# Kernel tuning notes

Measured on AMD Instinct MI355X. Metric: run time of the kernel, lower is better.

## Reference

```python
import jax, jax.numpy as jnp
import numpy as np

# NLMConv1DBlock: NLM LogicMachine(depth=2, breadth=2, input_dims=[0, inp_dim, 3],
# output_dims=[D,D,D], logic_hidden_dim=None -> each logic MLP is Linear+Sigmoid),
# followed by swish -> Conv1d(D, D, k=3, pad=1) over the t axis -> swish.
# Only the unary (arity-1) output of the second NLM layer is consumed, so the
# nullary/binary heads of layer 2 are never computed (their params are unused).


def swish(x):
    return x * jax.nn.sigmoid(x)


def lin_sig(x, W, b):
    # LogicInference with logic_hidden_dim=None: single Linear + Sigmoid
    return jax.nn.sigmoid(x @ W.T + b)


def reduce_unary(f1):
    # Reducer(dim=1): [B, n, C] -> [B, 2C]; exclude_self is a no-op for arity 1.
    # Channels interleaved as (exists_0, forall_0, exists_1, forall_1, ...)
    e = jnp.max(f1, axis=1)
    a = jnp.min(f1, axis=1)
    return jnp.stack([e, a], axis=-1).reshape(f1.shape[0], -1)


def reduce_pair(f2):
    # Reducer(dim=2, exclude_self=True): [B, n, n, C] -> [B, n, 2C].
    # Diagonal (i==j) masked to 0 for exists(max) and 1 for forall(min);
    # reduction over the second object index (axis=2). Interleaved exists/forall.
    n = f2.shape[1]
    eye = jnp.eye(n, dtype=bool)[None, :, :, None]
    e = jnp.max(jnp.where(eye, jnp.zeros((), f2.dtype), f2), axis=2)
    a = jnp.min(jnp.where(eye, jnp.ones((), f2.dtype), f2), axis=2)
    return jnp.stack([e, a], axis=-1).reshape(f2.shape[0], n, -1)


def perm2(f2):
    # Permutation(dim=2): concat identity and object-dim transpose along channels
    return jnp.concatenate([f2, jnp.swapaxes(f2, 1, 2)], axis=-1)


def setup_inputs() -> dict:
    key = jax.random.key(0)
    ks = jax.random.split(key, 12)
    b, t, n, inp_dim, D = 16, 16, 64, 2, 32
    s = 0.1
    x = jax.random.normal(ks[0], (b, t, n, inp_dim), jnp.float32)
    # Layer 1 logic MLPs (forward concat order: [expand, input, reduce])
    W1_0 = jax.random.normal(ks[1], (D, 2 * inp_dim), jnp.float32) * s        # nullary: reduce(unary) -> 2*inp_dim
    b1_0 = jax.random.normal(ks[2], (D,), jnp.float32) * s
    W1_1 = jax.random.normal(ks[3], (D, inp_dim + 6), jnp.float32) * s        # unary: [x, reduce(cmp)] -> inp_dim + 2*3
    b1_1 = jax.random.normal(ks[4], (D,), jnp.float32) * s
    W1_2 = jax.random.normal(ks[5], (D, 2 * (inp_dim + 3)), jnp.float32) * s  # binary: perm2([expand(x), cmp])
    b1_2 = jax.random.normal(ks[6], (D,), jnp.float32) * s
    # Layer 2, only the unary head is used downstream
    W2_1 = jax.random.normal(ks[7], (D, 4 * D), jnp.float32) * s              # [expand(g0), g1, reduce(g2)]
    b2_1 = jax.random.normal(ks[8], (D,), jnp.float32) * s
    # Conv1d(D, D, kernel_size=3, padding=1), OIH layout
    Wc = jax.random.normal(ks[9], (D, D, 3), jnp.float32) * s
    bc = jax.random.normal(ks[10], (D,), jnp.float32) * s
    return {"x": x, "W1_0": W1_0, "b1_0": b1_0, "W1_1": W1_1, "b1_1": b1_1,
            "W1_2": W1_2, "b1_2": b1_2, "W2_1": W2_1, "b2_1": b2_1,
            "Wc": Wc, "bc": bc}


def reference(x, W1_0, b1_0, W1_1, b1_1, W1_2, b1_2, W2_1, b2_1, Wc, bc):
    b, t, n, c = x.shape
    B = b * t
    xf = x.reshape(B, n, c)

    # pairwise relational inputs: [B, n, n, 3]
    ar = jnp.arange(n)
    base = jnp.stack([ar[:, None] < ar[None, :], ar[:, None] == ar[None, :]],
                     axis=-1).astype(x.dtype)                       # [n, n, 2], batch-invariant
    numbers = xf[:, :, 1]
    cmp3 = (numbers[:, :, None] < numbers[:, None, :]).astype(x.dtype)
    cmp = jnp.concatenate([jnp.broadcast_to(base[None], (B, n, n, 2)),
                           cmp3[..., None]], axis=-1)

    # --- NLM layer 1 (input dims [0, c, 3]) ---
    g0 = lin_sig(reduce_unary(xf), W1_0, b1_0)                                # [B, D]
    g1 = lin_sig(jnp.concatenate([xf, reduce_pair(cmp)], axis=-1), W1_1, b1_1)  # [B, n, D]
    f2 = jnp.concatenate([jnp.broadcast_to(xf[:, :, None, :], (B, n, n, c)), cmp], axis=-1)
    g2 = lin_sig(perm2(f2), W1_2, b1_2)                                       # [B, n, n, D]

    # --- NLM layer 2, unary head only (block takes nlm(...)[1]) ---
    D = g1.shape[-1]
    h1_in = jnp.concatenate([jnp.broadcast_to(g0[:, None, :], (B, n, D)),
                             g1, reduce_pair(g2)], axis=-1)                   # [B, n, 4D]
    h1 = swish(lin_sig(h1_in, W2_1, b2_1))                                    # [B, n, D]

    # (b t) n c -> (b n) c t, conv1d over t, -> b t n c, swish
    y = h1.reshape(b, t, n, D).transpose(0, 2, 3, 1).reshape(b * n, D, t)
    y = jax.lax.conv_general_dilated(y, Wc, (1,), [(1, 1)],
                                     dimension_numbers=('NCH', 'OIH', 'NCH'))
    y = y + bc[None, :, None]
    y = y.reshape(b, n, D, t).transpose(0, 3, 1, 2)
    return swish(y)
```

## Files before the change

kernel.cpp:

```cpp
#include <hip/hip_runtime.h>

#define NN 64
#define DD 32

__device__ __forceinline__ float sigmoidf_(float x) {
    return 1.0f / (1.0f + __expf(-x));
}

__global__ __launch_bounds__(1024) void stage1_kernel(
    const float* __restrict__ x,
    const float* __restrict__ W1_0, const float* __restrict__ b1_0,
    const float* __restrict__ W1_1, const float* __restrict__ b1_1,
    const float* __restrict__ W1_2, const float* __restrict__ b1_2,
    const float* __restrict__ W2_1, const float* __restrict__ b2_1,
    float* __restrict__ h1ws)
{
    __shared__ __align__(16) float sx0[NN];
    __shared__ __align__(16) float sx1[NN];
    __shared__ __align__(16) float sBvT[DD][68];
    __shared__ __align__(16) float sFeat[NN][100];
    __shared__ __align__(16) float sW2p[DD][100];
    __shared__ float sW12[DD*10];
    __shared__ float sB12[DD];
    __shared__ float sW11t[8*DD];
    __shared__ float sB11[DD];
    __shared__ float sG0[DD];
    __shared__ float sZ0[DD];
    __shared__ float sEC2[NN];
    __shared__ float sAC2[NN];

    const int tid = threadIdx.x;
    const int bb  = blockIdx.x;
    const int d   = tid & 31;

    if (tid < NN) {
        sx0[tid] = x[(bb*NN + tid)*2 + 0];
        sx1[tid] = x[(bb*NN + tid)*2 + 1];
    }
    for (int idx = tid; idx < DD*96; idx += 1024) {
        int dr = idx / 96, kp = idx - dr*96;
        sW2p[dr][kp] = W2_1[dr*128 + 32 + kp];
    }
    if (tid < 320) {
        sW12[tid] = W1_2[tid];
    } else if (tid < 352) {
        sB12[tid - 320] = b1_2[tid - 320];
    } else if (tid < 608) {
        int idx = tid - 352; int dr = idx >> 3, c = idx & 7;
        sW11t[c*DD + dr] = W1_1[idx];
    } else if (tid < 640) {
        sB11[tid - 608] = b1_1[tid - 608];
    }
    __syncthreads();

    const float w0 = sW12[d*10+0], w1 = sW12[d*10+1], w2 = sW12[d*10+2],
                w4 = sW12[d*10+4], w5 = sW12[d*10+5], w6 = sW12[d*10+6],
                w7 = sW12[d*10+7], w9 = sW12[d*10+9];
    const float bw = sB12[d];

    {
        int j = tid >> 5;
        sBvT[d][j]    = sx0[j]*w5 + sx1[j]*w6;
        sBvT[d][j+32] = sx0[j+32]*w5 + sx1[j+32]*w6;
    }
    if (tid < NN) {
        float ni = sx1[tid];
        float mx = -1e30f, mn = 1e30f;
        for (int j = 0; j < NN; ++j) {
            float nj = sx1[j];
            bool v = (j != tid);
            mx = fmaxf(mx, v ? nj : -1e30f);
            mn = fminf(mn, v ? nj :  1e30f);
        }
        sEC2[tid] = (ni < mx) ? 1.0f : 0.0f;
        sAC2[tid] = (ni < mn) ? 1.0f : 0.0f;
    } else if (tid < 96) {
        int dd = tid - 64;
        float mx0 = -1e30f, mn0 = 1e30f, mx1 = -1e30f, mn1 = 1e30f;
        for (int j = 0; j < NN; ++j) {
            float a = sx0[j], c = sx1[j];
            mx0 = fmaxf(mx0, a); mn0 = fminf(mn0, a);
            mx1 = fmaxf(mx1, c); mn1 = fminf(mn1, c);
        }
        float z = mx0*W1_0[dd*4+0] + mn0*W1_0[dd*4+1]
                + mx1*W1_0[dd*4+2] + mn1*W1_0[dd*4+3] + b1_0[dd];
        sG0[dd] = sigmoidf_(z);
    }
    __syncthreads();

    if (tid < 32) {
        float z = b2_1[tid];
        const float* wr = W2_1 + tid*128;
        #pragma unroll
        for (int k = 0; k < 32; ++k) z += sG0[k]*wr[k];
        sZ0[tid] = z;
    }

    {
        const int ia = tid >> 5;
        const int ib = ia + 32;
        const float na = sx1[ia], nb = sx1[ib];
        const float Aa = sx0[ia]*w0 + na*w1 + bw;
        const float Ab = sx0[ib]*w0 + nb*w1 + bw;
        const float A2a = Aa + w2, A7a = Aa + w7;
        const float A2b = Ab + w2, A7b = Ab + w7;
        float smaxa = -1e30f, smina = 1e30f;
        float smaxb = -1e30f, sminb = 1e30f;
        const float* bvrow = sBvT[d];

        #pragma unroll 4
        for (int jc = 0; jc < 8; ++jc) {
            const float4 bv4 = *(const float4*)(bvrow + jc*4);
            const float4 nj4 = *(const float4*)(&sx1[jc*4]);
            const float bva[4] = {bv4.x, bv4.y, bv4.z, bv4.w};
            const float nja[4] = {nj4.x, nj4.y, nj4.z, nj4.w};
            #pragma unroll
            for (int e = 0; e < 4; ++e) {
                const int j = jc*4 + e;
                float ta = ((ia < j) ? A2a : A7a) + bva[e];
                float qa = (na < nja[e]) ? w4 : 0.0f;
                qa       = (nja[e] < na) ? w9 : qa;
                ta += qa;
                const bool va = (j != ia);
                smaxa = fmaxf(smaxa, va ? ta : -1e30f);
                smina = fminf(smina, va ? ta :  1e30f);
                float tb = A7b + bva[e];
                float qb = (nb < nja[e]) ? w4 : 0.0f;
                qb       = (nja[e] < nb) ? w9 : qb;
                tb += qb;
                smaxb = fmaxf(smaxb, tb);
                sminb = fminf(sminb, tb);
            }
        }
        #pragma unroll 4
        for (int jc = 8; jc < 16; ++jc) {
            const float4 bv4 = *(const float4*)(bvrow + jc*4);
            const float4 nj4 = *(const float4*)(&sx1[jc*4]);
            const float bva[4] = {bv4.x, bv4.y, bv4.z, bv4.w};
            const float nja[4] = {nj4.x, nj4.y, nj4.z, nj4.w};
            #pragma unroll
            for (int e = 0; e < 4; ++e) {
                const int j = jc*4 + e;
                float ta = A2a + bva[e];
                float qa = (na < nja[e]) ? w4 : 0.0f;
                qa       = (nja[e] < na) ? w9 : qa;
                ta += qa;
                smaxa = fmaxf(smaxa, ta);
                smina = fminf(smina, ta);
                float tb = ((ib < j) ? A2b : A7b) + bva[e];
                float qb = (nb < nja[e]) ? w4 : 0.0f;
                qb       = (nja[e] < nb) ? w9 : qb;
                tb += qb;
                const bool vb = (j != ib);
                smaxb = fmaxf(smaxb, vb ? tb : -1e30f);
                sminb = fminf(sminb, vb ? tb :  1e30f);
            }
        }
        sFeat[ia][32 + 2*d] = sigmoidf_(smaxa);
        sFeat[ia][33 + 2*d] = sigmoidf_(smina);
        sFeat[ib][32 + 2*d] = sigmoidf_(smaxb);
        sFeat[ib][33 + 2*d] = sigmoidf_(sminb);

        float z1a = sx0[ia]*sW11t[0*DD+d] + na*sW11t[1*DD+d]
                  + ((ia < NN-1) ? sW11t[2*DD+d] : 0.0f)
                  + ((ia == 0)   ? sW11t[3*DD+d] : 0.0f)
                  + sEC2[ia]*sW11t[6*DD+d] + sAC2[ia]*sW11t[7*DD+d] + sB11[d];
        sFeat[ia][d] = sigmoidf_(z1a);
        float z1b = sx0[ib]*sW11t[0*DD+d] + nb*sW11t[1*DD+d]
                  + sW11t[2*DD+d]
                  - ((ib == NN-1) ? sW11t[2*DD+d] : 0.0f)
                  + sEC2[ib]*sW11t[6*DD+d] + sAC2[ib]*sW11t[7*DD+d] + sB11[d];
        sFeat[ib][d] = sigmoidf_(z1b);
    }
    __syncthreads();

    if (tid < 512) {
        const int i  = tid >> 4;
        const int dh = tid & 15;
        const float* fA = sFeat[i];
        const float* fB = sFeat[i+32];
        const float* wA = sW2p[dh];
        const float* wB = sW2p[dh+16];
        float a00 = sZ0[dh], a01 = sZ0[dh+16];
        float a10 = a00,     a11 = a01;
        #pragma unroll
        for (int kc = 0; kc < 96; kc += 4) {
            float4 fa = *(const float4*)(fA + kc);
            float4 fb = *(const float4*)(fB + kc);
            float4 pa = *(const float4*)(wA + kc);
            float4 pb = *(const float4*)(wB + kc);
            a00 += fa.x*pa.x + fa.y*pa.y + fa.z*pa.z + fa.w*pa.w;
            a01 += fa.x*pb.x + fa.y*pb.y + fa.z*pb.z + fa.w*pb.w;
            a10 += fb.x*pa.x + fb.y*pa.y + fb.z*pa.z + fb.w*pa.w;
            a11 += fb.x*pb.x + fb.y*pb.y + fb.z*pb.z + fb.w*pb.w;
        }
        float* orow = h1ws + bb*(NN*DD);
        float h;
        h = sigmoidf_(a00); orow[i*DD + dh]           = h * sigmoidf_(h);
        h = sigmoidf_(a01); orow[i*DD + dh + 16]      = h * sigmoidf_(h);
        h = sigmoidf_(a10); orow[(i+32)*DD + dh]      = h * sigmoidf_(h);
        h = sigmoidf_(a11); orow[(i+32)*DD + dh + 16] = h * sigmoidf_(h);
    }
}

__global__ __launch_bounds__(512) void conv_kernel(
    const float* __restrict__ h1ws,
    const float* __restrict__ Wc,
    const float* __restrict__ bc,
    float* __restrict__ out)
{
    __shared__ __align__(16) float sh[4][18][32];

    const int tid = threadIdx.x;
    const int blk = blockIdx.x;
    const int b   = blk >> 4;
    const int n0  = (blk & 15) * 4;
    const int t   = tid >> 5;
    const int dd  = tid & 31;

    float wreg[96];
    {
        const float* wrow = Wc + dd*96;
        #pragma unroll
        for (int c = 0; c < 24; ++c) {
            float4 v = *(const float4*)(wrow + c*4);
            wreg[c*4+0] = v.x; wreg[c*4+1] = v.y;
            wreg[c*4+2] = v.z; wreg[c*4+3] = v.w;
        }
    }
    for (int idx = tid; idx < 4*16*32; idx += 512) {
        int nl = idx >> 9; int rem = idx & 511;
        int tl = rem >> 5; int dl = rem & 31;
        sh[nl][tl+1][dl] = h1ws[((b*16 + tl)*NN + (n0+nl))*DD + dl];
    }
    if (tid < 256) {
        int nl = tid >> 6; int r = tid & 63;
        int row = (r >> 5) * 17; int dl = r & 31;
        sh[nl][row][dl] = 0.0f;
    }
    const float bcv = bc[dd];
    __syncthreads();

    #pragma unroll
    for (int g = 0; g < 4; ++g) {
        float acc = bcv;
        const float* r0 = &sh[g][t][0];
        const float* r1 = &sh[g][t+1][0];
        const float* r2 = &sh[g][t+2][0];
        #pragma unroll
        for (int c = 0; c < 8; ++c) {
            float4 f0  = *(const float4*)(r0 + c*4);
            float4 f1  = *(const float4*)(r1 + c*4);
            float4 f2v = *(const float4*)(r2 + c*4);
            const int q = c*12;
            acc += f0.x*wreg[q+0] + f1.x*wreg[q+1]  + f2v.x*wreg[q+2];
            acc += f0.y*wreg[q+3] + f1.y*wreg[q+4]  + f2v.y*wreg[q+5];
            acc += f0.z*wreg[q+6] + f1.z*wreg[q+7]  + f2v.z*wreg[q+8];
            acc += f0.w*wreg[q+9] + f1.w*wreg[q+10] + f2v.w*wreg[q+11];
        }
        out[((b*16 + t)*NN + (n0+g))*DD + dd] = acc * sigmoidf_(acc);
    }
}

extern "C" void kernel_launch(void* const* d_in, const int* in_sizes, int n_in,
                              void* d_out, int out_size, void* d_ws, size_t ws_size,
                              hipStream_t stream) {
    const float* x    = (const float*)d_in[0];
    const float* W1_0 = (const float*)d_in[1];
    const float* b1_0 = (const float*)d_in[2];
    const float* W1_1 = (const float*)d_in[3];
    const float* b1_1 = (const float*)d_in[4];
    const float* W1_2 = (const float*)d_in[5];
    const float* b1_2 = (const float*)d_in[6];
    const float* W2_1 = (const float*)d_in[7];
    const float* b2_1 = (const float*)d_in[8];
    const float* Wc   = (const float*)d_in[9];
    const float* bc   = (const float*)d_in[10];

    float* h1buf = (float*)d_out;
    float* out   = (float*)d_out;

    stage1_kernel<<<256, 1024, 0, stream>>>(x, W1_0, b1_0, W1_1, b1_1,
                                            W1_2, b1_2, W2_1, b2_1, h1buf);
    conv_kernel<<<256, 512, 0, stream>>>(h1buf, Wc, bc, out);
}
```

Baseline: 98.39 us.

## Broadcast object features via readlane and retile second-layer matmul to four rows

```diff
diff --git a/kernel.cpp b/kernel.cpp
--- a/kernel.cpp
+++ b/kernel.cpp
@@ -5,6 +5,10 @@
 
 __device__ __forceinline__ float sigmoidf_(float x) {
     return 1.0f / (1.0f + __expf(-x));
+}
+
+__device__ __forceinline__ float rlanef_(float v, int l) {
+    return __int_as_float(__builtin_amdgcn_readlane(__float_as_int(v), l));
 }
 
 __global__ __launch_bounds__(1024) void stage1_kernel(
@@ -17,7 +21,6 @@
 {
     __shared__ __align__(16) float sx0[NN];
     __shared__ __align__(16) float sx1[NN];
-    __shared__ __align__(16) float sBvT[DD][68];
     __shared__ __align__(16) float sFeat[NN][100];
     __shared__ __align__(16) float sW2p[DD][100];
     __shared__ float sW12[DD*10];
@@ -53,16 +56,14 @@
     }
     __syncthreads();
 
+    const float myx0 = sx0[tid & 63];
+    const float myx1 = sx1[tid & 63];
+
     const float w0 = sW12[d*10+0], w1 = sW12[d*10+1], w2 = sW12[d*10+2],
                 w4 = sW12[d*10+4], w5 = sW12[d*10+5], w6 = sW12[d*10+6],
                 w7 = sW12[d*10+7], w9 = sW12[d*10+9];
     const float bw = sB12[d];
 
-    {
-        int j = tid >> 5;
-        sBvT[d][j]    = sx0[j]*w5 + sx1[j]*w6;
-        sBvT[d][j+32] = sx0[j+32]*w5 + sx1[j+32]*w6;
-    }
     if (tid < NN) {
         float ni = sx1[tid];
         float mx = -1e30f, mn = 1e30f;
@@ -102,104 +103,99 @@
         const float na = sx1[ia], nb = sx1[ib];
         const float Aa = sx0[ia]*w0 + na*w1 + bw;
         const float Ab = sx0[ib]*w0 + nb*w1 + bw;
-        const float A2a = Aa + w2, A7a = Aa + w7;
-        const float A2b = Ab + w2, A7b = Ab + w7;
+        const float A24a = Aa + w2 + w4, A29a = Aa + w2 + w9;
+        const float A74a = Aa + w7 + w4, A79a = Aa + w7 + w9;
+        const float A24b = Ab + w2 + w4, A29b = Ab + w2 + w9;
+        const float A74b = Ab + w7 + w4, A79b = Ab + w7 + w9;
         float smaxa = -1e30f, smina = 1e30f;
         float smaxb = -1e30f, sminb = 1e30f;
-        const float* bvrow = sBvT[d];
-
-        #pragma unroll 4
-        for (int jc = 0; jc < 8; ++jc) {
-            const float4 bv4 = *(const float4*)(bvrow + jc*4);
-            const float4 nj4 = *(const float4*)(&sx1[jc*4]);
-            const float bva[4] = {bv4.x, bv4.y, bv4.z, bv4.w};
-            const float nja[4] = {nj4.x, nj4.y, nj4.z, nj4.w};
-            #pragma unroll
-            for (int e = 0; e < 4; ++e) {
-                const int j = jc*4 + e;
-                float ta = ((ia < j) ? A2a : A7a) + bva[e];
-                float qa = (na < nja[e]) ? w4 : 0.0f;
-                qa       = (nja[e] < na) ? w9 : qa;
-                ta += qa;
-                const bool va = (j != ia);
-                smaxa = fmaxf(smaxa, va ? ta : -1e30f);
-                smina = fminf(smina, va ? ta :  1e30f);
-                float tb = A7b + bva[e];
-                float qb = (nb < nja[e]) ? w4 : 0.0f;
-                qb       = (nja[e] < nb) ? w9 : qb;
-                tb += qb;
-                smaxb = fmaxf(smaxb, tb);
-                sminb = fminf(sminb, tb);
-            }
-        }
-        #pragma unroll 4
-        for (int jc = 8; jc < 16; ++jc) {
-            const float4 bv4 = *(const float4*)(bvrow + jc*4);
-            const float4 nj4 = *(const float4*)(&sx1[jc*4]);
-            const float bva[4] = {bv4.x, bv4.y, bv4.z, bv4.w};
-            const float nja[4] = {nj4.x, nj4.y, nj4.z, nj4.w};
-            #pragma unroll
-            for (int e = 0; e < 4; ++e) {
-                const int j = jc*4 + e;
-                float ta = A2a + bva[e];
-                float qa = (na < nja[e]) ? w4 : 0.0f;
-                qa       = (nja[e] < na) ? w9 : qa;
-                ta += qa;
-                smaxa = fmaxf(smaxa, ta);
-                smina = fminf(smina, ta);
-                float tb = ((ib < j) ? A2b : A7b) + bva[e];
-                float qb = (nb < nja[e]) ? w4 : 0.0f;
-                qb       = (nja[e] < nb) ? w9 : qb;
-                tb += qb;
-                const bool vb = (j != ib);
-                smaxb = fmaxf(smaxb, vb ? tb : -1e30f);
-                sminb = fminf(sminb, vb ? tb :  1e30f);
-            }
-        }
-        sFeat[ia][32 + 2*d] = sigmoidf_(smaxa);
-        sFeat[ia][33 + 2*d] = sigmoidf_(smina);
-        sFeat[ib][32 + 2*d] = sigmoidf_(smaxb);
-        sFeat[ib][33 + 2*d] = sigmoidf_(sminb);
+
+        #pragma unroll
+        for (int j = 0; j < 32; ++j) {
+            const float x0j = rlanef_(myx0, j);
+            const float x1j = rlanef_(myx1, j);
+            const float bv  = x0j*w5 + x1j*w6;
+            const float tb = ((nb < x1j) ? A74b : A79b) + bv;
+            smaxb = fmaxf(smaxb, tb);
+            sminb = fminf(sminb, tb);
+            const bool ca = (na < x1j);
+            const float t2 = ca ? A24a : A29a;
+            const float t7 = ca ? A74a : A79a;
+            const float ta = ((ia < j) ? t2 : t7) + bv;
+            const bool va = (j != ia);
+            smaxa = fmaxf(smaxa, va ? ta : -1e30f);
+            smina = fminf(smina, va ? ta :  1e30f);
+        }
+        #pragma unroll
+        for (int j = 32; j < 64; ++j) {
+            const float x0j = rlanef_(myx0, j);
+            const float x1j = rlanef_(myx1, j);
+            const float bv  = x0j*w5 + x1j*w6;
+            const float ta = ((na < x1j) ? A24a : A29a) + bv;
+            smaxa = fmaxf(smaxa, ta);
+            smina = fminf(smina, ta);
+            const bool cb = (nb < x1j);
+            const float t2 = cb ? A24b : A29b;
+            const float t7 = cb ? A74b : A79b;
+            const float tb = ((ib < j) ? t2 : t7) + bv;
+            const bool vb = (j != ib);
+            smaxb = fmaxf(smaxb, vb ? tb : -1e30f);
+            sminb = fminf(sminb, vb ? tb :  1e30f);
+        }
+        *(float2*)&sFeat[ia][32 + 2*d] = make_float2(sigmoidf_(smaxa), sigmoidf_(smina));
+        *(float2*)&sFeat[ib][32 + 2*d] = make_float2(sigmoidf_(smaxb), sigmoidf_(sminb));
 
         float z1a = sx0[ia]*sW11t[0*DD+d] + na*sW11t[1*DD+d]
-                  + ((ia < NN-1) ? sW11t[2*DD+d] : 0.0f)
-                  + ((ia == 0)   ? sW11t[3*DD+d] : 0.0f)
+                  + sW11t[2*DD+d]
+                  + ((ia == 0) ? sW11t[3*DD+d] : 0.0f)
                   + sEC2[ia]*sW11t[6*DD+d] + sAC2[ia]*sW11t[7*DD+d] + sB11[d];
         sFeat[ia][d] = sigmoidf_(z1a);
         float z1b = sx0[ib]*sW11t[0*DD+d] + nb*sW11t[1*DD+d]
-                  + sW11t[2*DD+d]
-                  - ((ib == NN-1) ? sW11t[2*DD+d] : 0.0f)
+                  + ((ib < NN-1) ? sW11t[2*DD+d] : 0.0f)
                   + sEC2[ib]*sW11t[6*DD+d] + sAC2[ib]*sW11t[7*DD+d] + sB11[d];
         sFeat[ib][d] = sigmoidf_(z1b);
     }
     __syncthreads();
 
-    if (tid < 512) {
-        const int i  = tid >> 4;
+    if (tid < 256) {
+        const int i0 = tid >> 4;
         const int dh = tid & 15;
-        const float* fA = sFeat[i];
-        const float* fB = sFeat[i+32];
+        const float* f0 = sFeat[i0];
+        const float* f1 = sFeat[i0+16];
+        const float* f2 = sFeat[i0+32];
+        const float* f3 = sFeat[i0+48];
         const float* wA = sW2p[dh];
         const float* wB = sW2p[dh+16];
-        float a00 = sZ0[dh], a01 = sZ0[dh+16];
-        float a10 = a00,     a11 = a01;
+        const float z0A = sZ0[dh], z0B = sZ0[dh+16];
+        float a0A = z0A, a0B = z0B, a1A = z0A, a1B = z0B;
+        float a2A = z0A, a2B = z0B, a3A = z0A, a3B = z0B;
         #pragma unroll
         for (int kc = 0; kc < 96; kc += 4) {
-            float4 fa = *(const float4*)(fA + kc);
-            float4 fb = *(const float4*)(fB + kc);
-            float4 pa = *(const float4*)(wA + kc);
-            float4 pb = *(const float4*)(wB + kc);
-            a00 += fa.x*pa.x + fa.y*pa.y + fa.z*pa.z + fa.w*pa.w;
-            a01 += fa.x*pb.x + fa.y*pb.y + fa.z*pb.z + fa.w*pb.w;
-            a10 += fb.x*pa.x + fb.y*pa.y + fb.z*pa.z + fb.w*pa.w;
-            a11 += fb.x*pb.x + fb.y*pb.y + fb.z*pb.z + fb.w*pb.w;
+            const float4 pa = *(const float4*)(wA + kc);
+            const float4 pb = *(const float4*)(wB + kc);
+            const float4 v0 = *(const float4*)(f0 + kc);
+            const float4 v1 = *(const float4*)(f1 + kc);
+            const float4 v2 = *(const float4*)(f2 + kc);
+            const float4 v3 = *(const float4*)(f3 + kc);
+            a0A += v0.x*pa.x + v0.y*pa.y + v0.z*pa.z + v0.w*pa.w;
+            a0B += v0.x*pb.x + v0.y*pb.y + v0.z*pb.z + v0.w*pb.w;
+            a1A += v1.x*pa.x + v1.y*pa.y + v1.z*pa.z + v1.w*pa.w;
+            a1B += v1.x*pb.x + v1.y*pb.y + v1.z*pb.z + v1.w*pb.w;
+            a2A += v2.x*pa.x + v2.y*pa.y + v2.z*pa.z + v2.w*pa.w;
+            a2B += v2.x*pb.x + v2.y*pb.y + v2.z*pb.z + v2.w*pb.w;
+            a3A += v3.x*pa.x + v3.y*pa.y + v3.z*pa.z + v3.w*pa.w;
+            a3B += v3.x*pb.x + v3.y*pb.y + v3.z*pb.z + v3.w*pb.w;
         }
         float* orow = h1ws + bb*(NN*DD);
         float h;
-        h = sigmoidf_(a00); orow[i*DD + dh]           = h * sigmoidf_(h);
-        h = sigmoidf_(a01); orow[i*DD + dh + 16]      = h * sigmoidf_(h);
-        h = sigmoidf_(a10); orow[(i+32)*DD + dh]      = h * sigmoidf_(h);
-        h = sigmoidf_(a11); orow[(i+32)*DD + dh + 16] = h * sigmoidf_(h);
+        h = sigmoidf_(a0A); orow[ i0     *DD + dh]      = h * sigmoidf_(h);
+        h = sigmoidf_(a0B); orow[ i0     *DD + dh + 16] = h * sigmoidf_(h);
+        h = sigmoidf_(a1A); orow[(i0+16)*DD + dh]       = h * sigmoidf_(h);
+        h = sigmoidf_(a1B); orow[(i0+16)*DD + dh + 16]  = h * sigmoidf_(h);
+        h = sigmoidf_(a2A); orow[(i0+32)*DD + dh]       = h * sigmoidf_(h);
+        h = sigmoidf_(a2B); orow[(i0+32)*DD + dh + 16]  = h * sigmoidf_(h);
+        h = sigmoidf_(a3A); orow[(i0+48)*DD + dh]       = h * sigmoidf_(h);
+        h = sigmoidf_(a3B); orow[(i0+48)*DD + dh + 16]  = h * sigmoidf_(h);
     }
 }
 
```

Result: no change. 97.56 us (-0.8%).
